# Performance work log

Hardware: AMD Instinct MI355X
Metric: run time of the kernel (lower is better)

Reference implementation:

```python
import jax, jax.numpy as jnp
import numpy as np

T, B, E, H = 1024, 8, 1024, 16
DH = E // H
MASKED_BIAS = -10000.0


def setup_inputs() -> dict:
    key = jax.random.key(0)
    k1, k2, k3 = jax.random.split(key, 3)
    query = jax.random.normal(k1, (T, B, E), dtype=jnp.float32)
    # xavier-uniform-ish scale for the fused QKV and output projections
    qkv_w = jax.random.normal(k2, (3 * E, E), dtype=jnp.float32) * (1.0 / np.sqrt(2.0 * E))
    out_w = jax.random.normal(k3, (E, E), dtype=jnp.float32) * (1.0 / np.sqrt(E))
    return {
        "query": query,
        "qkv_w": qkv_w,
        "qkv_b": jnp.zeros((3 * E,), jnp.float32),
        "out_w": out_w,
        "out_b": jnp.zeros((E,), jnp.float32),
    }


def reference(query, qkv_w, qkv_b, out_w, out_b):
    # query: [T, B, E] (Time x Batch x Channel, fairseq convention)
    tgt_len, bsz, embed_dim = query.shape
    scaling = DH ** (-0.5)

    # Fused QKV projection (QuantLinear fake-quant treated as identity numerics)
    qkv = jnp.einsum("tbe,fe->tbf", query, qkv_w) + qkv_b  # [T, B, 3E]
    q, k, v = jnp.split(qkv, 3, axis=-1)
    q = q * scaling

    def to_heads(x):  # [T, B, E] -> [B*H, T, DH]
        return x.reshape(tgt_len, bsz * H, DH).transpose(1, 0, 2)

    q, k, v = to_heads(q), to_heads(k), to_heads(v)

    # attn_weights: [B*H, T, S]
    attn_weights = jnp.einsum("ntd,nsd->nts", q, k)

    # causal mask from the tril `bias` buffer with masked_bias fill
    causal = jnp.tril(jnp.ones((tgt_len, tgt_len), dtype=bool))
    attn_weights = jnp.where(causal[None, :, :], attn_weights,
                             jnp.asarray(MASKED_BIAS, attn_weights.dtype))

    attn_probs = jax.nn.softmax(attn_weights, axis=-1)
    # dropout p=0.0 in eval: no-op

    attn = jnp.einsum("nts,nsd->ntd", attn_probs, v)  # [B*H, T, DH]
    attn = attn.transpose(1, 0, 2).reshape(tgt_len, bsz, embed_dim)  # [T, B, E]

    out = jnp.einsum("tbe,fe->tbf", attn, out_w) + out_b
    return out
```

## Files before the change

kernel.cpp:

```cpp
#include <hip/hip_runtime.h>

typedef __attribute__((ext_vector_type(4))) float f32x4;
typedef __attribute__((ext_vector_type(16))) float f32x16;
typedef __attribute__((ext_vector_type(8))) short bf16x8;
typedef __attribute__((ext_vector_type(4))) unsigned short u16x4;
typedef __attribute__((ext_vector_type(4))) unsigned int u32x4;

#define T_DIM 1024
#define B_DIM 8
#define E_DIM 1024
#define H_DIM 16
#define DH 64

__device__ __forceinline__ unsigned short f2bf(float f) {
  unsigned int u = __builtin_bit_cast(unsigned int, f);
  u += 0x7fffu + ((u >> 16) & 1u);
  return (unsigned short)(u >> 16);
}

__device__ __forceinline__ unsigned int cvtpk_bf16(float lo, float hi) {
  unsigned int r;
  asm("v_cvt_pk_bf16_f32 %0, %1, %2" : "=v"(r) : "v"(lo), "v"(hi));
  return r;
}

__device__ __forceinline__ float exp2_hw(float x) {
  float r;
  asm("v_exp_f32 %0, %1" : "=v"(r) : "v"(x));
  return r;
}

__device__ __forceinline__ f32x4 mfma16(bf16x8 a, bf16x8 b, f32x4 c) {
  return __builtin_amdgcn_mfma_f32_16x16x32_bf16(a, b, c, 0, 0, 0);
}
__device__ __forceinline__ f32x16 mfma32(bf16x8 a, bf16x8 b, f32x16 c) {
  return __builtin_amdgcn_mfma_f32_32x32x16_bf16(a, b, c, 0, 0, 0);
}

__global__ __launch_bounds__(256) void cast_all(
    const float* __restrict__ q, const float* __restrict__ w1,
    const float* __restrict__ w2, unsigned short* __restrict__ dq,
    unsigned short* __restrict__ dw1, unsigned short* __restrict__ dw2) {
  int i = blockIdx.x * 256 + threadIdx.x;
  const float* src;
  unsigned short* dst;
  int off;
  if (i < 2097152)      { src = q;  dst = dq;  off = i; }
  else if (i < 2883584) { src = w1; dst = dw1; off = i - 2097152; }
  else                  { src = w2; dst = dw2; off = i - 2883584; }
  f32x4 v = *(const f32x4*)(src + (size_t)off * 4);
  u16x4 o;
  o[0] = f2bf(v[0]); o[1] = f2bf(v[1]); o[2] = f2bf(v[2]); o[3] = f2bf(v[3]);
  *(u16x4*)(dst + (size_t)off * 4) = o;
}

__device__ __forceinline__ void mainloop_128x256(
    const unsigned short* __restrict__ Ab,
    const unsigned short* __restrict__ Bb,
    unsigned short* smem, f32x4 acc[4][4]) {
  const int tid = threadIdx.x;
  const int wave = tid >> 6, lane = tid & 63;
  const int lr = lane & 15, lg = lane >> 4;
  const int x7 = lr & 7;
  const int wr = wave >> 2, wc = wave & 3;
  const int rlo = lane >> 3;
  const int csw = 8 * ((lane & 7) ^ rlo);

#define STG(KT, BUF)                                                            \
  {                                                                             \
    unsigned short* la_ = smem + (BUF) * 24576;                                 \
    unsigned short* lb_ = la_ + 8192;                                           \
    _Pragma("unroll")                                                           \
    for (int c_ = 0; c_ < 2; ++c_) {                                            \
      const int ins_ = wave * 2 + c_;                                           \
      __builtin_amdgcn_global_load_lds(                                         \
          (const __attribute__((address_space(1))) void*)(Ab + (size_t)(ins_ * 8 + rlo) * 1024 + (KT) * 64 + csw), \
          (__attribute__((address_space(3))) void*)(la_ + ins_ * 512), 16, 0, 0); \
    }                                                                           \
    _Pragma("unroll")                                                           \
    for (int c_ = 0; c_ < 4; ++c_) {                                            \
      const int ins_ = wave * 4 + c_;                                           \
      __builtin_amdgcn_global_load_lds(                                         \
          (const __attribute__((address_space(1))) void*)(Bb + (size_t)(ins_ * 8 + rlo) * 1024 + (KT) * 64 + csw), \
          (__attribute__((address_space(3))) void*)(lb_ + ins_ * 512), 16, 0, 0); \
    }                                                                           \
  }

#define COMPUTE(BUF)                                                            \
  {                                                                             \
    const unsigned short* la_ = smem + (BUF) * 24576;                           \
    const unsigned short* ha_ = la_ + (wr * 64) * 64;                           \
    const unsigned short* hb_ = la_ + 8192 + (wc * 64) * 64;                    \
    _Pragma("unroll")                                                           \
    for (int ks_ = 0; ks_ < 2; ++ks_) {                                         \
      bf16x8 af_[4], bf_[4];                                                    \
      const int cu_ = (((ks_ * 4 + lg) ^ x7) << 3);                             \
      _Pragma("unroll")                                                         \
      for (int i_ = 0; i_ < 4; ++i_) {                                          \
        af_[i_] = *(const bf16x8*)(ha_ + (i_ * 16 + lr) * 64 + cu_);            \
        bf_[i_] = *(const bf16x8*)(hb_ + (i_ * 16 + lr) * 64 + cu_);            \
      }                                                                         \
      __builtin_amdgcn_s_setprio(1);                                            \
      _Pragma("unroll")                                                         \
      for (int mi_ = 0; mi_ < 4; ++mi_)                                         \
        _Pragma("unroll")                                                       \
        for (int ni_ = 0; ni_ < 4; ++ni_)                                       \
          acc[mi_][ni_] = mfma16(af_[mi_], bf_[ni_], acc[mi_][ni_]);            \
      __builtin_amdgcn_s_setprio(0);                                            \
    }                                                                           \
  }

#define ENDT(WAITSTR)                                                           \
  asm volatile("s_waitcnt " WAITSTR ::: "memory");                              \
  __builtin_amdgcn_s_barrier();                                                 \
  __builtin_amdgcn_sched_barrier(0);

  STG(0, 0) STG(1, 1)
  ENDT("vmcnt(6)")

  for (int tt = 0; tt < 12; tt += 3) {
    STG(tt + 2, 2) COMPUTE(0) ENDT("vmcnt(6)")
    STG(tt + 3, 0) COMPUTE(1) ENDT("vmcnt(6)")
    STG(tt + 4, 1) COMPUTE(2) ENDT("vmcnt(6)")
  }
  STG(14, 2) COMPUTE(0) ENDT("vmcnt(6)")
  STG(15, 0) COMPUTE(1) ENDT("vmcnt(6)")
  COMPUTE(2) ENDT("vmcnt(0)")
  COMPUTE(0)
#undef STG
#undef COMPUTE
#undef ENDT
}

__global__ __launch_bounds__(512) void gemm_qkv12(
    const unsigned short* __restrict__ A, const unsigned short* __restrict__ W,
    const float* __restrict__ bias,
    unsigned short* __restrict__ Qh, unsigned short* __restrict__ Kh,
    unsigned short* __restrict__ Vh) {
  extern __shared__ unsigned short smem[];
  const int bid = blockIdx.x;
  const int xcd = bid & 7, i = bid >> 3;
  const int m0 = (xcd * 8 + (i & 7)) * 128;
  const int n0 = (i >> 3) * 256;

  f32x4 acc[4][4];
  const f32x4 z4 = {0.f, 0.f, 0.f, 0.f};
#pragma unroll
  for (int a = 0; a < 4; ++a)
#pragma unroll
    for (int b2 = 0; b2 < 4; ++b2) acc[a][b2] = z4;

  mainloop_128x256(A + (size_t)m0 * 1024, W + (size_t)n0 * 1024, smem, acc);

  const int lane = threadIdx.x & 63, wave = threadIdx.x >> 6;
  const int lr = lane & 15, lg = lane >> 4;
  const int wr = wave >> 2, wc = wave & 3;
#pragma unroll
  for (int mf = 0; mf < 4; ++mf)
#pragma unroll
    for (int nf = 0; nf < 4; ++nf)
#pragma unroll
      for (int j = 0; j < 4; ++j) {
        int m = m0 + wr * 64 + mf * 16 + lg * 4 + j;
        int f = n0 + wc * 64 + nf * 16 + lr;
        float v = acc[mf][nf][j] + bias[f];
        int t = m >> 3, b = m & 7;
        int e = f & 1023, h = e >> 6, d = e & 63;
        int which = f >> 10;
        size_t idx = ((size_t)(b * 16 + h) * T_DIM + t) * DH + d;
        if (which == 0)      Qh[idx] = f2bf(v * 0.18033688011111772f);
        else if (which == 1) Kh[idx] = f2bf(v);
        else                 Vh[idx] = f2bf(v);
      }
}

__global__ __launch_bounds__(512) void gemm_out12(
    const unsigned short* __restrict__ A, const unsigned short* __restrict__ W,
    const float* __restrict__ bias, float* __restrict__ out) {
  extern __shared__ unsigned short smem[];
  const int bid = blockIdx.x;
  const int xcd = bid & 7, i = bid >> 3;
  const int m0 = (xcd * 8 + (i & 7)) * 128;
  const int n0 = (i >> 3) * 256;

  f32x4 acc[4][4];
  const f32x4 z4 = {0.f, 0.f, 0.f, 0.f};
#pragma unroll
  for (int a = 0; a < 4; ++a)
#pragma unroll
    for (int b2 = 0; b2 < 4; ++b2) acc[a][b2] = z4;

  mainloop_128x256(A + (size_t)m0 * 1024, W + (size_t)n0 * 1024, smem, acc);

  const int lane = threadIdx.x & 63, wave = threadIdx.x >> 6;
  const int lr = lane & 15, lg = lane >> 4;
  const int wr = wave >> 2, wc = wave & 3;
#pragma unroll
  for (int mf = 0; mf < 4; ++mf)
#pragma unroll
    for (int nf = 0; nf < 4; ++nf)
#pragma unroll
      for (int j = 0; j < 4; ++j) {
        int m = m0 + wr * 64 + mf * 16 + lg * 4 + j;
        int f = n0 + wc * 64 + nf * 16 + lr;
        out[(size_t)m * E_DIM + f] = acc[mf][nf][j] + bias[f];
      }
}

__global__ __launch_bounds__(256) void transpose_v(
    const unsigned short* __restrict__ Vh, unsigned short* __restrict__ Vt) {
  __shared__ unsigned short tile[64][72];
  const int n = blockIdx.x, t0 = blockIdx.y * 64;
  const int tid = threadIdx.x;
  const int r = tid >> 3, c8 = tid & 7;
#pragma unroll
  for (int it = 0; it < 2; ++it) {
    int row = it * 32 + r;
    bf16x8 v = *(const bf16x8*)(Vh + ((size_t)n * T_DIM + t0 + row) * DH + c8 * 8);
    *(bf16x8*)&tile[row][c8 * 8] = v;
  }
  __syncthreads();
#pragma unroll
  for (int it = 0; it < 2; ++it) {
    int d = it * 32 + r;
    bf16x8 ov;
#pragma unroll
    for (int jj = 0; jj < 8; ++jj) ov[jj] = (short)tile[c8 * 8 + jj][d];
    *(bf16x8*)(Vt + ((size_t)n * DH + d) * T_DIM + t0 + c8 * 8) = ov;
  }
}

__global__ __launch_bounds__(256) void flash_attn6(
    const unsigned short* __restrict__ Qh, const unsigned short* __restrict__ Kh,
    const unsigned short* __restrict__ Vt, unsigned short* __restrict__ attn) {
  __shared__ unsigned short lds[2][2][4096];
  const int tid = threadIdx.x;
  const int wave = tid >> 6, lane = tid & 63;
  const int lq = lane & 31, hi = lane >> 5;
  const int bid = blockIdx.x;
  const int qt = 7 - (bid >> 7);
  const int n = bid & 127;
  const int b = n >> 4, h = n & 15;
  const int q0w = qt * 128 + wave * 32;
  const int q = q0w + lq;
  const int nbb = 2 * qt + 2;
  const int mynb = (q0w + 95) >> 6;

  const unsigned short* kh_n = Kh + (size_t)n * (T_DIM * DH);
  const unsigned short* vt_n = Vt + (size_t)n * (DH * T_DIM);

  const int rlo = lane >> 3;
  const int csw = 8 * ((lane & 7) ^ rlo);

#define STAGE(S0, BUF)                                                          \
  {                                                                             \
    _Pragma("unroll")                                                           \
    for (int m_ = 0; m_ < 2; ++m_) {                                            \
      const int instr_ = wave * 2 + m_;                                         \
      const int r_ = instr_ * 8 + rlo;                                          \
      __builtin_amdgcn_global_load_lds(                                         \
          (const __attribute__((address_space(1))) void*)(kh_n + (size_t)((S0) + r_) * DH + csw), \
          (__attribute__((address_space(3))) void*)(&lds[BUF][0][instr_ * 512]), 16, 0, 0); \
      __builtin_amdgcn_global_load_lds(                                         \
          (const __attribute__((address_space(1))) void*)(vt_n + (size_t)r_ * T_DIM + (S0) + csw), \
          (__attribute__((address_space(3))) void*)(&lds[BUF][1][instr_ * 512]), 16, 0, 0); \
    }                                                                           \
  }

  bf16x8 qf[4];
  const unsigned short* qp = Qh + ((size_t)n * T_DIM + q) * DH + hi * 8;
#pragma unroll
  for (int kk = 0; kk < 4; ++kk) qf[kk] = *(const bf16x8*)(qp + kk * 16);

  f32x16 o0, o1;
#pragma unroll
  for (int r = 0; r < 16; ++r) { o0[r] = 0.f; o1[r] = 0.f; }
  float m_run = -1e30f, l_run = 0.f;

  STAGE(0, 0);
  asm volatile("s_waitcnt vmcnt(0)");
  __builtin_amdgcn_s_barrier();

  const int swzr = (lq & 7) << 4;

  for (int i = 0; i < nbb; ++i) {
    const int cur = i & 1;
    if (i + 1 < nbb) {
      STAGE((i + 1) * 64, cur ^ 1);
      asm volatile("s_waitcnt vmcnt(4)");
    } else {
      asm volatile("s_waitcnt vmcnt(0)");
    }
    __builtin_amdgcn_s_barrier();
    __builtin_amdgcn_sched_barrier(0);

    if (i < mynb) {
      const int s0 = i * 64;
      const unsigned short* kb = lds[cur][0];
      const unsigned short* vb = lds[cur][1];
      f32x16 sA, sB;
#pragma unroll
      for (int r = 0; r < 16; ++r) { sA[r] = 0.f; sB[r] = 0.f; }
      __builtin_amdgcn_s_setprio(1);
#pragma unroll
      for (int kk = 0; kk < 4; ++kk) {
        const int cb = ((kk * 32 + hi * 16) ^ swzr) >> 1;
        bf16x8 ka = *(const bf16x8*)(kb + lq * 64 + cb);
        bf16x8 kbf = *(const bf16x8*)(kb + (32 + lq) * 64 + cb);
        sA = mfma32(ka, qf[kk], sA);
        sB = mfma32(kbf, qf[kk], sB);
      }
      __builtin_amdgcn_s_setprio(0);
      if (i == mynb - 1) {
#pragma unroll
        for (int r = 0; r < 16; ++r) {
          int sp = s0 + (r & 3) + 8 * (r >> 2) + 4 * hi;
          if (sp > q)      sA[r] = -10000.0f;
          if (sp + 32 > q) sB[r] = -10000.0f;
        }
      }
      float t0 = fmaxf(sA[0], sB[0]), t1 = fmaxf(sA[1], sB[1]);
      float t2 = fmaxf(sA[2], sB[2]), t3 = fmaxf(sA[3], sB[3]);
#pragma unroll
      for (int r = 4; r < 16; r += 4) {
        t0 = fmaxf(t0, fmaxf(sA[r], sB[r]));
        t1 = fmaxf(t1, fmaxf(sA[r + 1], sB[r + 1]));
        t2 = fmaxf(t2, fmaxf(sA[r + 2], sB[r + 2]));
        t3 = fmaxf(t3, fmaxf(sA[r + 3], sB[r + 3]));
      }
      float tmax = fmaxf(fmaxf(t0, t1), fmaxf(t2, t3));
      tmax = fmaxf(tmax, __shfl_xor(tmax, 32));
      if (__any(tmax - m_run > 11.5f)) {
        float m_new = fmaxf(m_run, tmax);
        float sc = exp2_hw(m_run - m_new);
        l_run *= sc;
#pragma unroll
        for (int r = 0; r < 16; ++r) { o0[r] *= sc; o1[r] *= sc; }
        m_run = m_new;
      }
      float r0 = 0.f, r1 = 0.f, r2 = 0.f, r3 = 0.f;
#pragma unroll
      for (int r = 0; r < 16; r += 4) {
        sA[r] = exp2_hw(sA[r] - m_run);         r0 += sA[r];
        sA[r + 1] = exp2_hw(sA[r + 1] - m_run); r1 += sA[r + 1];
        sA[r + 2] = exp2_hw(sA[r + 2] - m_run); r2 += sA[r + 2];
        sA[r + 3] = exp2_hw(sA[r + 3] - m_run); r3 += sA[r + 3];
      }
#pragma unroll
      for (int r = 0; r < 16; r += 4) {
        sB[r] = exp2_hw(sB[r] - m_run);         r0 += sB[r];
        sB[r + 1] = exp2_hw(sB[r + 1] - m_run); r1 += sB[r + 1];
        sB[r + 2] = exp2_hw(sB[r + 2] - m_run); r2 += sB[r + 2];
        sB[r + 3] = exp2_hw(sB[r + 3] - m_run); r3 += sB[r + 3];
      }
      float rs = (r0 + r1) + (r2 + r3);
      rs += __shfl_xor(rs, 32);
      l_run += rs;
      unsigned int pk[16];
#pragma unroll
      for (int ii = 0; ii < 8; ++ii) pk[ii]     = cvtpk_bf16(sA[2 * ii], sA[2 * ii + 1]);
#pragma unroll
      for (int ii = 0; ii < 8; ++ii) pk[8 + ii] = cvtpk_bf16(sB[2 * ii], sB[2 * ii + 1]);
      __builtin_amdgcn_s_setprio(1);
#pragma unroll
      for (int ks = 0; ks < 4; ++ks) {
        unsigned int A0 = pk[ks * 4 + 0], A1 = pk[ks * 4 + 1];
        unsigned int B0 = pk[ks * 4 + 2], B1 = pk[ks * 4 + 3];
        unsigned int xA0 = __shfl_xor(A0, 32), xA1 = __shfl_xor(A1, 32);
        unsigned int xB0 = __shfl_xor(B0, 32), xB1 = __shfl_xor(B1, 32);
        u32x4 uu;
        uu[0] = hi ? xB0 : A0;
        uu[1] = hi ? xB1 : A1;
        uu[2] = hi ? B0 : xA0;
        uu[3] = hi ? B1 : xA1;
        bf16x8 pf = __builtin_bit_cast(bf16x8, uu);
        const int cb = ((ks * 32 + hi * 16) ^ swzr) >> 1;
        bf16x8 v0 = *(const bf16x8*)(vb + lq * 64 + cb);
        bf16x8 v1 = *(const bf16x8*)(vb + (32 + lq) * 64 + cb);
        o0 = mfma32(v0, pf, o0);
        o1 = mfma32(v1, pf, o1);
      }
      __builtin_amdgcn_s_setprio(0);
    }
    __builtin_amdgcn_s_barrier();
  }
#undef STAGE

  const float inv = 1.0f / l_run;
  unsigned short* op = attn + ((size_t)q * B_DIM + b) * E_DIM + h * DH;
#pragma unroll
  for (int g = 0; g < 4; ++g) {
    u16x4 w0, w1;
#pragma unroll
    for (int jj = 0; jj < 4; ++jj) {
      w0[jj] = f2bf(o0[g * 4 + jj] * inv);
      w1[jj] = f2bf(o1[g * 4 + jj] * inv);
    }
    int d = 8 * g + 4 * hi;
    *(u16x4*)(op + d) = w0;
    *(u16x4*)(op + 32 + d) = w1;
  }
}

extern "C" void kernel_launch(void* const* d_in, const int* in_sizes, int n_in,
                              void* d_out, int out_size, void* d_ws, size_t ws_size,
                              hipStream_t stream) {
  const float* query = (const float*)d_in[0];
  const float* qkv_w = (const float*)d_in[1];
  const float* qkv_b = (const float*)d_in[2];
  const float* out_w = (const float*)d_in[3];
  const float* out_b = (const float*)d_in[4];
  float* out = (float*)d_out;

  char* ws = (char*)d_ws;
  unsigned short* Abf  = (unsigned short*)(ws);
  unsigned short* Wbf  = (unsigned short*)(ws + (size_t)(16u << 20));
  unsigned short* OWbf = (unsigned short*)(ws + (size_t)(22u << 20));
  unsigned short* Qh   = (unsigned short*)(ws + (size_t)(24u << 20));
  unsigned short* Kh   = (unsigned short*)(ws + (size_t)(40u << 20));
  unsigned short* Vh   = (unsigned short*)(ws + (size_t)(56u << 20));
  unsigned short* Vt   = (unsigned short*)(ws + (size_t)(72u << 20));
  unsigned short* attn = Abf;

  cast_all<<<12288, 256, 0, stream>>>(query, qkv_w, out_w, Abf, Wbf, OWbf);
  gemm_qkv12<<<768, 512, 147456, stream>>>(Abf, Wbf, qkv_b, Qh, Kh, Vh);
  transpose_v<<<dim3(128, 16), 256, 0, stream>>>(Vh, Vt);
  flash_attn6<<<1024, 256, 0, stream>>>(Qh, Kh, Vt, attn);
  gemm_out12<<<256, 512, 147456, stream>>>(attn, OWbf, out_b, out);
}
```

Baseline: 157.1 us.

## Shrink GEMM tiles to 128x128 with 4 waves and double-buffered LDS

Both projection GEMMs move from 128x256 tiles with 8 waves and a triple-buffered, dynamically sized LDS pipeline to 128x128 tiles with 4 waves and a static 64KB double buffer. Each block stays in lockstep through two barriers per k-step. The grid doubles (1536 and 512 blocks), which gives the out projection more blocks to fill the CUs and lets several blocks share a CU. The cost is lower operand reuse per block, more global/L2 traffic, and a shallower prefetch pipeline with extra barriers.

```diff
diff --git a/kernel.cpp b/kernel.cpp
--- a/kernel.cpp
+++ b/kernel.cpp
@@ -54,7 +54,7 @@
   *(u16x4*)(dst + (size_t)off * 4) = o;
 }
 
-__device__ __forceinline__ void mainloop_128x256(
+__device__ __forceinline__ void mainloop_128x128v2(
     const unsigned short* __restrict__ Ab,
     const unsigned short* __restrict__ Bb,
     unsigned short* smem, f32x4 acc[4][4]) {
@@ -62,25 +62,21 @@
   const int wave = tid >> 6, lane = tid & 63;
   const int lr = lane & 15, lg = lane >> 4;
   const int x7 = lr & 7;
-  const int wr = wave >> 2, wc = wave & 3;
+  const int wr = wave >> 1, wc = wave & 1;
   const int rlo = lane >> 3;
   const int csw = 8 * ((lane & 7) ^ rlo);
 
 #define STG(KT, BUF)                                                            \
   {                                                                             \
-    unsigned short* la_ = smem + (BUF) * 24576;                                 \
+    unsigned short* la_ = smem + (BUF) * 16384;                                 \
     unsigned short* lb_ = la_ + 8192;                                           \
-    _Pragma("unroll")                                                           \
-    for (int c_ = 0; c_ < 2; ++c_) {                                            \
-      const int ins_ = wave * 2 + c_;                                           \
-      __builtin_amdgcn_global_load_lds(                                         \
-          (const __attribute__((address_space(1))) void*)(Ab + (size_t)(ins_ * 8 + rlo) * 1024 + (KT) * 64 + csw), \
-          (__attribute__((address_space(3))) void*)(la_ + ins_ * 512), 16, 0, 0); \
-    }                                                                           \
     _Pragma("unroll")                                                           \
     for (int c_ = 0; c_ < 4; ++c_) {                                            \
       const int ins_ = wave * 4 + c_;                                           \
       __builtin_amdgcn_global_load_lds(                                         \
+          (const __attribute__((address_space(1))) void*)(Ab + (size_t)(ins_ * 8 + rlo) * 1024 + (KT) * 64 + csw), \
+          (__attribute__((address_space(3))) void*)(la_ + ins_ * 512), 16, 0, 0); \
+      __builtin_amdgcn_global_load_lds(                                         \
           (const __attribute__((address_space(1))) void*)(Bb + (size_t)(ins_ * 8 + rlo) * 1024 + (KT) * 64 + csw), \
           (__attribute__((address_space(3))) void*)(lb_ + ins_ * 512), 16, 0, 0); \
     }                                                                           \
@@ -88,7 +84,7 @@
 
 #define COMPUTE(BUF)                                                            \
   {                                                                             \
-    const unsigned short* la_ = smem + (BUF) * 24576;                           \
+    const unsigned short* la_ = smem + (BUF) * 16384;                           \
     const unsigned short* ha_ = la_ + (wr * 64) * 64;                           \
     const unsigned short* hb_ = la_ + 8192 + (wc * 64) * 64;                    \
     _Pragma("unroll")                                                           \
@@ -110,38 +106,39 @@
     }                                                                           \
   }
 
-#define ENDT(WAITSTR)                                                           \
-  asm volatile("s_waitcnt " WAITSTR ::: "memory");                              \
-  __builtin_amdgcn_s_barrier();                                                 \
+  STG(0, 0)
+  asm volatile("s_waitcnt vmcnt(0)" ::: "memory");
+  __builtin_amdgcn_s_barrier();
   __builtin_amdgcn_sched_barrier(0);
 
-  STG(0, 0) STG(1, 1)
-  ENDT("vmcnt(6)")
-
-  for (int tt = 0; tt < 12; tt += 3) {
-    STG(tt + 2, 2) COMPUTE(0) ENDT("vmcnt(6)")
-    STG(tt + 3, 0) COMPUTE(1) ENDT("vmcnt(6)")
-    STG(tt + 4, 1) COMPUTE(2) ENDT("vmcnt(6)")
-  }
-  STG(14, 2) COMPUTE(0) ENDT("vmcnt(6)")
-  STG(15, 0) COMPUTE(1) ENDT("vmcnt(6)")
-  COMPUTE(2) ENDT("vmcnt(0)")
-  COMPUTE(0)
+#pragma unroll 2
+  for (int t = 0; t < 16; ++t) {
+    if (t < 15) {
+      STG(t + 1, (t + 1) & 1)
+      asm volatile("s_waitcnt vmcnt(8)" ::: "memory");
+    } else {
+      asm volatile("s_waitcnt vmcnt(0)" ::: "memory");
+    }
+    __builtin_amdgcn_s_barrier();
+    __builtin_amdgcn_sched_barrier(0);
+    COMPUTE(t & 1)
+    __builtin_amdgcn_s_barrier();
+    __builtin_amdgcn_sched_barrier(0);
+  }
 #undef STG
 #undef COMPUTE
-#undef ENDT
-}
-
-__global__ __launch_bounds__(512) void gemm_qkv12(
+}
+
+__global__ __launch_bounds__(256) void gemm_qkv13(
     const unsigned short* __restrict__ A, const unsigned short* __restrict__ W,
     const float* __restrict__ bias,
     unsigned short* __restrict__ Qh, unsigned short* __restrict__ Kh,
     unsigned short* __restrict__ Vh) {
-  extern __shared__ unsigned short smem[];
+  __shared__ unsigned short smem[32768];
   const int bid = blockIdx.x;
   const int xcd = bid & 7, i = bid >> 3;
   const int m0 = (xcd * 8 + (i & 7)) * 128;
-  const int n0 = (i >> 3) * 256;
+  const int n0 = (i >> 3) * 128;
 
   f32x4 acc[4][4];
   const f32x4 z4 = {0.f, 0.f, 0.f, 0.f};
@@ -150,11 +147,11 @@
 #pragma unroll
     for (int b2 = 0; b2 < 4; ++b2) acc[a][b2] = z4;
 
-  mainloop_128x256(A + (size_t)m0 * 1024, W + (size_t)n0 * 1024, smem, acc);
+  mainloop_128x128v2(A + (size_t)m0 * 1024, W + (size_t)n0 * 1024, smem, acc);
 
   const int lane = threadIdx.x & 63, wave = threadIdx.x >> 6;
   const int lr = lane & 15, lg = lane >> 4;
-  const int wr = wave >> 2, wc = wave & 3;
+  const int wr = wave >> 1, wc = wave & 1;
 #pragma unroll
   for (int mf = 0; mf < 4; ++mf)
 #pragma unroll
@@ -174,14 +171,14 @@
       }
 }
 
-__global__ __launch_bounds__(512) void gemm_out12(
+__global__ __launch_bounds__(256) void gemm_out13(
     const unsigned short* __restrict__ A, const unsigned short* __restrict__ W,
     const float* __restrict__ bias, float* __restrict__ out) {
-  extern __shared__ unsigned short smem[];
+  __shared__ unsigned short smem[32768];
   const int bid = blockIdx.x;
   const int xcd = bid & 7, i = bid >> 3;
   const int m0 = (xcd * 8 + (i & 7)) * 128;
-  const int n0 = (i >> 3) * 256;
+  const int n0 = (i >> 3) * 128;
 
   f32x4 acc[4][4];
   const f32x4 z4 = {0.f, 0.f, 0.f, 0.f};
@@ -190,11 +187,11 @@
 #pragma unroll
     for (int b2 = 0; b2 < 4; ++b2) acc[a][b2] = z4;
 
-  mainloop_128x256(A + (size_t)m0 * 1024, W + (size_t)n0 * 1024, smem, acc);
+  mainloop_128x128v2(A + (size_t)m0 * 1024, W + (size_t)n0 * 1024, smem, acc);
 
   const int lane = threadIdx.x & 63, wave = threadIdx.x >> 6;
   const int lr = lane & 15, lg = lane >> 4;
-  const int wr = wave >> 2, wc = wave & 3;
+  const int wr = wave >> 1, wc = wave & 1;
 #pragma unroll
   for (int mf = 0; mf < 4; ++mf)
 #pragma unroll
@@ -423,8 +420,8 @@
   unsigned short* attn = Abf;
 
   cast_all<<<12288, 256, 0, stream>>>(query, qkv_w, out_w, Abf, Wbf, OWbf);
-  gemm_qkv12<<<768, 512, 147456, stream>>>(Abf, Wbf, qkv_b, Qh, Kh, Vh);
+  gemm_qkv13<<<1536, 256, 0, stream>>>(Abf, Wbf, qkv_b, Qh, Kh, Vh);
   transpose_v<<<dim3(128, 16), 256, 0, stream>>>(Vh, Vt);
   flash_attn6<<<1024, 256, 0, stream>>>(Qh, Kh, Vt, attn);
-  gemm_out12<<<256, 512, 147456, stream>>>(attn, OWbf, out_b, out);
-}
+  gemm_out13<<<512, 256, 0, stream>>>(attn, OWbf, out_b, out);
+}
```

New measurement: 155.6 us. No clear change (-0.9%).
